# Performance work log

Hardware: AMD Instinct MI355X
Metric: run time of the kernel (lower is better)

Reference implementation:

```python
import jax, jax.numpy as jnp
import numpy as np

T, N, G, H, COV, TW, E = 96, 1024, 128, 512, 8, 8, 32768
D2 = TW * (TW - 1)          # 56, GNN summary width
IN = COV + D2               # 64, exogenous input width


def setup_inputs() -> dict:
    key = jax.random.key(0)
    ks = jax.random.split(key, 32)
    s = 1.0 / np.sqrt(H)

    def u(k, shape):
        return jax.random.uniform(k, shape, jnp.float32, -s, s)

    inp = {
        "input": jax.random.normal(ks[0], (T, 1, IN), jnp.float32),
        "x_nodes": jax.random.normal(ks[1], (T, N, N), jnp.float32),
        "edge_index": jax.random.randint(ks[2], (T, 2, E), 0, N, dtype=jnp.int64),
        "W1": u(ks[3], (N, G)), "b1": u(ks[4], (G,)),
        "W2": u(ks[5], (G, G)), "b2": u(ks[6], (G,)),
        "Wfc": u(ks[7], (G * N, D2)), "bfc": u(ks[8], (D2,)),
        "W_ii": u(ks[9], (IN, H)), "W_gi": u(ks[10], (D2, H)), "W_hi": u(ks[11], (H, H)), "b_i": u(ks[12], (H,)),
        "W_if": u(ks[13], (IN, H)), "W_gf": u(ks[14], (D2, H)), "W_hf": u(ks[15], (H, H)), "b_f": u(ks[16], (H,)),
        "W_ig": u(ks[17], (IN, H)), "W_gg": u(ks[18], (D2, H)), "W_hg": u(ks[19], (H, H)), "b_g": u(ks[20], (H,)),
        "W_io": u(ks[21], (IN, H)), "W_go": u(ks[22], (D2, H)), "W_ho": u(ks[23], (H, H)), "b_o": u(ks[24], (H,)),
    }
    return inp


def reference(input, x_nodes, edge_index,
              W1, b1, W2, b2, Wfc, bfc,
              W_ii, W_gi, W_hi, b_i,
              W_if, W_gf, W_hf, b_f,
              W_ig, W_gg, W_hg, b_g,
              W_io, W_go, W_ho, b_o):
    self_loops = jnp.arange(N, dtype=edge_index.dtype)

    def gcn_conv(x, src, dst, dinv, W, b):
        # GCNConv: out[dst] += d^-1/2[src] d^-1/2[dst] * (x @ W)[src], plus bias
        xw = x @ W                                   # [N, F_out]
        norm = dinv[src] * dinv[dst]                 # [E+N]
        msg = xw[src] * norm[:, None]
        return jax.ops.segment_sum(msg, dst, num_segments=N) + b

    def step(carry, inputs):
        h, c = carry
        x_t, xg, ei = inputs                         # [1,IN], [N,N], [2,E]
        src = jnp.concatenate([ei[0], self_loops])   # add self-loops
        dst = jnp.concatenate([ei[1], self_loops])
        deg = jax.ops.segment_sum(jnp.ones(src.shape, jnp.float32), dst, num_segments=N)
        dinv = jnp.where(deg > 0, jax.lax.rsqrt(jnp.maximum(deg, 1.0)), 0.0)

        xh = jax.nn.relu(gcn_conv(xg, src, dst, dinv, W1, b1))
        xh = gcn_conv(xh, src, dst, dinv, W2, b2)    # [N, G]
        g = jax.nn.relu(xh.reshape(1, -1) @ Wfc + bfc)  # [1, D2]

        i = jax.nn.sigmoid(x_t @ W_ii + g @ W_gi + h @ W_hi + b_i)
        f = jax.nn.sigmoid(x_t @ W_if + g @ W_gf + h @ W_hf + b_f)
        gt = jnp.tanh(x_t @ W_ig + g @ W_gg + h @ W_hg + b_g)
        o = jax.nn.sigmoid(x_t @ W_io + g @ W_go + h @ W_ho + b_o)
        c = f * c + i * gt
        h = o * jnp.tanh(c)
        return (h, c), h

    h0 = jnp.zeros((1, H), jnp.float32)
    c0 = jnp.zeros((1, H), jnp.float32)
    (h, c), outputs = jax.lax.scan(step, (h0, c0), (input, x_nodes, edge_index))
    return outputs, h, c
```

## Files before the change

### kernel.cpp

```cpp
#include <hip/hip_runtime.h>
#include <stdint.h>

#define T_    96
#define TC_   48
#define N_    1024
#define G_    128
#define H_    512
#define E_    32768
#define EN_   33792
#define D2_   56
#define IN_   64
#define KFC_  131072

typedef __bf16 bf16_t;
typedef __bf16 bf16x8 __attribute__((ext_vector_type(8)));
typedef float  f32x4  __attribute__((ext_vector_type(4)));
typedef unsigned short u16;
typedef unsigned long long u64;

struct PtrQuadF { const float* p[4]; };

__device__ inline bf16x8 cvt8(const float* p) {
    const f32x4 a0 = *(const f32x4*)p;
    const f32x4 a1 = *(const f32x4*)(p + 4);
    bf16x8 r;
    r[0] = (bf16_t)a0[0]; r[1] = (bf16_t)a0[1]; r[2] = (bf16_t)a0[2]; r[3] = (bf16_t)a0[3];
    r[4] = (bf16_t)a1[0]; r[5] = (bf16_t)a1[1]; r[6] = (bf16_t)a1[2]; r[7] = (bf16_t)a1[3];
    return r;
}


__global__ __launch_bounds__(1024) void build_kernel(const int* __restrict__ ei,
                                                     int* __restrict__ rowptr_g, int* __restrict__ deg_g,
                                                     u64* __restrict__ ecv) {
    int t = blockIdx.x, tid = threadIdx.x;
    __shared__ int sdeg[N_];
    __shared__ int sa[N_], sb[N_];
    __shared__ int sfill[N_];
    __shared__ float sdinv[N_];
    sdeg[tid] = 0;
    __syncthreads();
    const int* src_p = ei + (size_t)t * 2 * E_;
    const int* dst_p = src_p + E_;
    for (int e = tid; e < E_; e += 1024) atomicAdd(&sdeg[dst_p[e]], 1);
    __syncthreads();
    int d = sdeg[tid] + 1;
    sa[tid] = d;
    __syncthreads();
    int* cur = sa; int* nxt = sb;
    for (int off = 1; off < N_; off <<= 1) {
        int v = cur[tid];
        if (tid >= off) v += cur[tid - off];
        nxt[tid] = v;
        __syncthreads();
        int* tmp = cur; cur = nxt; nxt = tmp;
    }
    int start = cur[tid] - d + t * EN_;
    rowptr_g[t * N_ + tid] = start;
    deg_g[t * N_ + tid] = d;
    sfill[tid] = start;
    sdinv[tid] = rsqrtf((float)d);
    __syncthreads();
    for (int e = tid; e < EN_; e += 1024) {
        int s, dd;
        if (e < E_) { s = src_p[e]; dd = dst_p[e]; }
        else        { s = dd = e - E_; }
        float nrm = sdinv[s] * sdinv[dd];
        int pos = atomicAdd(&sfill[dd], 1);
        ecv[pos] = ((u64)__float_as_uint(nrm) << 32) | (unsigned int)s;
    }
}


__global__ __launch_bounds__(256) void transpose_kernel(const float* __restrict__ src, bf16_t* __restrict__ dst,
                                                        int R, int C, int Cpad) {
    __shared__ bf16_t tile[64][65];
    int rb = blockIdx.x * 64, cb = blockIdx.y * 64;
    int tx = threadIdx.x & 63, ty = threadIdx.x >> 6;
#pragma unroll
    for (int i = 0; i < 16; i++) {
        int r = rb + ty * 16 + i;
        int c = cb + tx;
        float v = 0.f;
        if (r < R && c < C) v = src[(size_t)r * C + c];
        tile[ty * 16 + i][tx] = (bf16_t)v;
    }
    __syncthreads();
#pragma unroll
    for (int i = 0; i < 16; i++) {
        int c = cb + ty * 16 + i;
        int r = rb + tx;
        if (c < Cpad && r < R) dst[(size_t)c * R + r] = tile[tx][ty * 16 + i];
    }
}


__global__ __launch_bounds__(256) void whcvt_kernel(PtrQuadF Wh, bf16_t* __restrict__ dst) {
    int g = blockIdx.y;
    int idx = blockIdx.x * 256 + threadIdx.x;
    dst[(size_t)g * H_ * H_ + idx] = (bf16_t)Wh.p[g][idx];
}


template<bool AF32>
__global__ __launch_bounds__(256) void gemm_g(const void* __restrict__ Ap, const bf16_t* __restrict__ B,
                                              bf16_t* __restrict__ C, const float* __restrict__ bias, int relu,
                                              int K, int Mtiles, size_t sA, size_t sC, int ldc) {
    int t = blockIdx.y;
    int mi = blockIdx.x % Mtiles, ni = blockIdx.x / Mtiles;
    int tid = threadIdx.x;
    int w = tid >> 6, l = tid & 63;
    int wm = w & 1, wn = w >> 1;
    int lm = l & 15, lq = l >> 4;
    f32x4 acc[4][4] = {};
    size_t aO = sA * t + (size_t)(mi * 128 + wm * 64 + lm) * K + lq * 8;
    const bf16_t* Ab16 = (const bf16_t*)Ap + aO;
    const float*  Ab32 = (const float*)Ap + aO;
    const bf16_t* Bb = B + (size_t)(ni * 128 + wn * 64 + lm) * K + lq * 8;
    for (int k0 = 0; k0 < K; k0 += 32) {
        bf16x8 af[4], bfv[4];
#pragma unroll
        for (int i = 0; i < 4; i++) {
            if (AF32) af[i] = cvt8(Ab32 + (size_t)i * 16 * K + k0);
            else      af[i] = *(const bf16x8*)(Ab16 + (size_t)i * 16 * K + k0);
        }
#pragma unroll
        for (int i = 0; i < 4; i++) bfv[i] = *(const bf16x8*)(Bb + (size_t)i * 16 * K + k0);
#pragma unroll
        for (int mt = 0; mt < 4; mt++)
#pragma unroll
            for (int nt = 0; nt < 4; nt++)
                acc[mt][nt] = __builtin_amdgcn_mfma_f32_16x16x32_bf16(af[mt], bfv[nt], acc[mt][nt], 0, 0, 0);
    }
#pragma unroll
    for (int mt = 0; mt < 4; mt++)
#pragma unroll
        for (int nt = 0; nt < 4; nt++) {
            int colg = ni * 128 + wn * 64 + nt * 16 + lm;
            float bv = bias ? bias[colg] : 0.f;
#pragma unroll
            for (int r = 0; r < 4; r++) {
                int row = mi * 128 + wm * 64 + mt * 16 + lq * 4 + r;
                float v = acc[mt][nt][r] + bv;
                if (relu) v = fmaxf(v, 0.f);
                C[sC * t + (size_t)row * ldc + colg] = (bf16_t)v;
            }
        }
}


__device__ inline void spmm_acc(u64 q, const bf16_t* Fb, int l, float& a0, float& a1) {
    int c = (int)(unsigned int)q;
    float wn = __uint_as_float((unsigned int)(q >> 32));
    unsigned int pk = *(const unsigned int*)(Fb + (size_t)c * 128 + 2 * l);
    a0 += wn * __uint_as_float(pk << 16);
    a1 += wn * __uint_as_float(pk & 0xffff0000u);
}

__global__ __launch_bounds__(256) void spmm_kernel(const int* __restrict__ rowptr, const int* __restrict__ deg,
                                                   const u64* __restrict__ ecv, const bf16_t* __restrict__ F,
                                                   const float* __restrict__ bias, int relu,
                                                   bf16_t* __restrict__ out, int t0) {
    int tl = blockIdx.y, t = t0 + tl;
    int w = threadIdx.x >> 6, l = threadIdx.x & 63;
    int r = blockIdx.x * 4 + w;
    int start = rowptr[t * N_ + r];
    int n = deg[t * N_ + r];
    const bf16_t* Fb = F + (size_t)tl * N_ * 128;
    const u64* ep = ecv + start;
    float a0 = 0.f, a1 = 0.f;
    int e = 0;
    for (; e + 4 <= n; e += 4) {
        u64 q0 = ep[e], q1 = ep[e + 1], q2 = ep[e + 2], q3 = ep[e + 3];
        spmm_acc(q0, Fb, l, a0, a1);
        spmm_acc(q1, Fb, l, a0, a1);
        spmm_acc(q2, Fb, l, a0, a1);
        spmm_acc(q3, Fb, l, a0, a1);
    }
    for (; e < n; e++) spmm_acc(ep[e], Fb, l, a0, a1);
    float v0 = a0 + bias[2 * l], v1 = a1 + bias[2 * l + 1];
    if (relu) { v0 = fmaxf(v0, 0.f); v1 = fmaxf(v1, 0.f); }
    bf16_t b0 = (bf16_t)v0, b1 = (bf16_t)v1;
    unsigned int po = (unsigned int)*(u16*)&b0 | ((unsigned int)*(u16*)&b1 << 16);
    *(unsigned int*)((u16*)(out + ((size_t)tl * N_ + r) * 128) + 2 * l) = po;
}


__global__ __launch_bounds__(256) void gfc_kernel(const bf16_t* __restrict__ XH2, const bf16_t* __restrict__ WfcT,
                                                  float* __restrict__ g_acc, int t0) {
    int tid = threadIdx.x;
    int w = tid >> 6, l = tid & 63;
    int lm = l & 15, lq = l >> 4;
    int n = w * 16 + lm;
    size_t k0 = (size_t)blockIdx.x * 1024;
    f32x4 acc[3] = {};
    const bf16_t* Ab = XH2 + (size_t)lm * KFC_ + k0 + lq * 8;
    const bf16_t* Bb = WfcT + (size_t)n * KFC_ + k0 + lq * 8;
    for (int ks = 0; ks < 32; ks++) {
        bf16x8 bfr = *(const bf16x8*)(Bb + ks * 32);
#pragma unroll
        for (int mt = 0; mt < 3; mt++) {
            bf16x8 a = *(const bf16x8*)(Ab + (size_t)(mt * 16) * KFC_ + ks * 32);
            acc[mt] = __builtin_amdgcn_mfma_f32_16x16x32_bf16(a, bfr, acc[mt], 0, 0, 0);
        }
    }
#pragma unroll
    for (int mt = 0; mt < 3; mt++)
#pragma unroll
        for (int r = 0; r < 4; r++) {
            int t = t0 + mt * 16 + lq * 4 + r;
            if (n < D2_) atomicAdd(&g_acc[t * 64 + n], acc[mt][r]);
        }
}


__global__ __launch_bounds__(512) void pregate_kernel(const float* __restrict__ xin, const float* __restrict__ g_acc,
                                                      const float* __restrict__ bfc,
                                                      PtrQuadF Wi, PtrQuadF Wg, PtrQuadF Wb,
                                                      float* __restrict__ out) {
    int gate = blockIdx.x, t = blockIdx.y, j = threadIdx.x;
    __shared__ float gl[D2_];
    __shared__ float xl[IN_];
    if (j < D2_) gl[j] = fmaxf(g_acc[t * 64 + j] + bfc[j], 0.f);
    if (j < IN_) xl[j] = xin[t * IN_ + j];
    __syncthreads();
    const float* wi = Wi.p[gate];
    const float* wg = Wg.p[gate];
    float acc = Wb.p[gate][j];
#pragma unroll 4
    for (int k = 0; k < IN_; k++) acc += xl[k] * wi[k * H_ + j];
#pragma unroll 4
    for (int k = 0; k < D2_; k++) acc += gl[k] * wg[k * H_ + j];
    out[(t * 4 + gate) * H_ + j] = acc;
}


__global__ __launch_bounds__(256) void lstm_kernel(const bf16_t* __restrict__ Whb, const float* __restrict__ pregate,
                                                   u64* __restrict__ h_slot, float* __restrict__ out) {
    int tid = threadIdx.x, bid = blockIdx.x;
    int jl = tid >> 3, kc = tid & 7;
    int j = bid * 32 + jl;
    int k0 = kc * 64;

    uint32_t w[128];
#pragma unroll
    for (int g4 = 0; g4 < 4; g4++) {
        const bf16_t* W = Whb + (size_t)g4 * H_ * H_;
#pragma unroll
        for (int m = 0; m < 32; m++) {
            int k = k0 + 2 * m;
            uint32_t lo = *(const u16*)(W + (size_t)k * H_ + j);
            uint32_t hi = *(const u16*)(W + (size_t)(k + 1) * H_ + j);
            w[g4 * 32 + m] = lo | (hi << 16);
        }
    }

    __shared__ __align__(16) float hl[H_];
    hl[tid] = 0.f;
    hl[tid + 256] = 0.f;
    float c = 0.f;
    __syncthreads();

    for (int step = 0; step < 96; step++) {
        float p0 = 0.f, p1 = 0.f, p2 = 0.f, p3 = 0.f;
        if (kc == 0) {
            const float* pre = pregate + (size_t)step * (4 * H_);
            p0 = pre[0 * H_ + j]; p1 = pre[1 * H_ + j];
            p2 = pre[2 * H_ + j]; p3 = pre[3 * H_ + j];
        }

        float s0 = 0.f, s1 = 0.f, s2 = 0.f, s3 = 0.f;
        const float4* h4 = (const float4*)(hl + k0);
#pragma unroll
        for (int q = 0; q < 16; q++) {
            float4 hq = h4[q];
#pragma unroll
            for (int p = 0; p < 2; p++) {
                float h0 = p ? hq.z : hq.x;
                float h1 = p ? hq.w : hq.y;
                int mi = q * 2 + p;
                uint32_t wv;
                wv = w[0 * 32 + mi];
                s0 += __uint_as_float(wv << 16) * h0 + __uint_as_float(wv & 0xffff0000u) * h1;
                wv = w[1 * 32 + mi];
                s1 += __uint_as_float(wv << 16) * h0 + __uint_as_float(wv & 0xffff0000u) * h1;
                wv = w[2 * 32 + mi];
                s2 += __uint_as_float(wv << 16) * h0 + __uint_as_float(wv & 0xffff0000u) * h1;
                wv = w[3 * 32 + mi];
                s3 += __uint_as_float(wv << 16) * h0 + __uint_as_float(wv & 0xffff0000u) * h1;
            }
        }
        s0 += __shfl_xor(s0, 1); s0 += __shfl_xor(s0, 2); s0 += __shfl_xor(s0, 4);
        s1 += __shfl_xor(s1, 1); s1 += __shfl_xor(s1, 2); s1 += __shfl_xor(s1, 4);
        s2 += __shfl_xor(s2, 1); s2 += __shfl_xor(s2, 2); s2 += __shfl_xor(s2, 4);
        s3 += __shfl_xor(s3, 1); s3 += __shfl_xor(s3, 2); s3 += __shfl_xor(s3, 4);

        if (kc == 0) {
            float ig = 1.f / (1.f + __expf(-(s0 + p0)));
            float fg = 1.f / (1.f + __expf(-(s1 + p1)));
            float gg = tanhf(s2 + p2);
            float og = 1.f / (1.f + __expf(-(s3 + p3)));
            c = fg * c + ig * gg;
            float h = og * tanhf(c);
            if (step < 95) {
                u64 v = ((u64)(unsigned int)(step + 1) << 32) | (u64)__float_as_uint(h);
                __hip_atomic_store(&h_slot[(size_t)step * H_ + j], v, __ATOMIC_RELAXED, __HIP_MEMORY_SCOPE_AGENT);
            }
            out[step * H_ + j] = h;
            if (step == 95) {
                out[96 * H_ + j] = h;
                out[97 * H_ + j] = c;
            }
        }
        if (step < 95) {
            __syncthreads();
            if (tid < 64) {
                unsigned int want = (unsigned int)(step + 1);
                const u64* base = h_slot + (size_t)step * H_ + tid * 8;
                u64 v[8];
                int need = 0xff;
                while (need) {
#pragma unroll
                    for (int s = 0; s < 8; s++)
                        if (need & (1 << s))
                            v[s] = __hip_atomic_load(&base[s], __ATOMIC_RELAXED, __HIP_MEMORY_SCOPE_AGENT);
                    int nd = 0;
#pragma unroll
                    for (int s = 0; s < 8; s++)
                        if ((need & (1 << s)) && (unsigned int)(v[s] >> 32) != want) nd |= 1 << s;
                    need = nd;
                    if (need) __builtin_amdgcn_s_sleep(1);
                }
                float4 f0, f1;
                f0.x = __uint_as_float((unsigned int)v[0]); f0.y = __uint_as_float((unsigned int)v[1]);
                f0.z = __uint_as_float((unsigned int)v[2]); f0.w = __uint_as_float((unsigned int)v[3]);
                f1.x = __uint_as_float((unsigned int)v[4]); f1.y = __uint_as_float((unsigned int)v[5]);
                f1.z = __uint_as_float((unsigned int)v[6]); f1.w = __uint_as_float((unsigned int)v[7]);
                ((float4*)hl)[tid * 2] = f0;
                ((float4*)hl)[tid * 2 + 1] = f1;
            }
            __syncthreads();
        }
    }
}


extern "C" void kernel_launch(void* const* d_in, const int* in_sizes, int n_in,
                              void* d_out, int out_size, void* d_ws, size_t ws_size,
                              hipStream_t stream) {
    const float* xin    = (const float*)d_in[0];
    const float* xnodes = (const float*)d_in[1];
    const int*   ei     = (const int*)d_in[2];
    const float* W1  = (const float*)d_in[3];
    const float* b1  = (const float*)d_in[4];
    const float* W2  = (const float*)d_in[5];
    const float* b2  = (const float*)d_in[6];
    const float* Wfc = (const float*)d_in[7];
    const float* bfc = (const float*)d_in[8];

    PtrQuadF Wi = {{(const float*)d_in[9],  (const float*)d_in[13], (const float*)d_in[17], (const float*)d_in[21]}};
    PtrQuadF Wg = {{(const float*)d_in[10], (const float*)d_in[14], (const float*)d_in[18], (const float*)d_in[22]}};
    PtrQuadF Wh = {{(const float*)d_in[11], (const float*)d_in[15], (const float*)d_in[19], (const float*)d_in[23]}};
    PtrQuadF Wb = {{(const float*)d_in[12], (const float*)d_in[16], (const float*)d_in[20], (const float*)d_in[24]}};

    char* ws = (char*)d_ws;
    size_t off = 0;
    auto alloc = [&](size_t bytes) { void* p = ws + off; off += (bytes + 255) & ~(size_t)255; return p; };

    bf16_t* C1      = (bf16_t*)alloc((size_t)TC_ * N_ * 128 * 2);
    bf16_t* XH1     = (bf16_t*)alloc((size_t)TC_ * N_ * 128 * 2);
    bf16_t* C2      = (bf16_t*)alloc((size_t)TC_ * N_ * 128 * 2);
    bf16_t* XH2     = (bf16_t*)alloc((size_t)TC_ * N_ * 128 * 2);
    u64*    ecv     = (u64*)   alloc((size_t)T_ * EN_ * 8);
    int*    deg     = (int*)   alloc((size_t)T_ * N_ * 4);
    int*    rowptr  = (int*)   alloc((size_t)T_ * N_ * 4);
    bf16_t* W1t     = (bf16_t*)alloc((size_t)128 * 1024 * 2);
    bf16_t* W2t     = (bf16_t*)alloc((size_t)128 * 128 * 2);
    bf16_t* WfcT    = (bf16_t*)alloc((size_t)64 * KFC_ * 2);
    bf16_t* Whb     = (bf16_t*)alloc((size_t)4 * H_ * H_ * 2);
    float*  g_acc   = (float*) alloc((size_t)T_ * 64 * 4);
    float*  pregate = (float*) alloc((size_t)T_ * 4 * H_ * 4);
    u64*    h_slot  = (u64*)   alloc((size_t)T_ * H_ * 8);

    hipMemsetAsync(g_acc, 0, (size_t)T_ * 64 * 4, stream);

    build_kernel<<<T_, 1024, 0, stream>>>(ei, rowptr, deg, ecv);

    transpose_kernel<<<dim3(16, 2), 256, 0, stream>>>(W1, W1t, 1024, 128, 128);
    transpose_kernel<<<dim3(2, 2), 256, 0, stream>>>(W2, W2t, 128, 128, 128);
    transpose_kernel<<<dim3(2048, 1), 256, 0, stream>>>(Wfc, WfcT, KFC_, D2_, 64);
    whcvt_kernel<<<dim3(1024, 4), 256, 0, stream>>>(Wh, Whb);

    for (int c = 0; c < T_ / TC_; c++) {
        int t0 = c * TC_;
        gemm_g<true><<<dim3(8, TC_), 256, 0, stream>>>(
            xnodes + (size_t)t0 * N_ * N_, W1t, C1, nullptr, 0,
            1024, 8, (size_t)N_ * N_, (size_t)N_ * 128, 128);
        spmm_kernel<<<dim3(256, TC_), 256, 0, stream>>>(rowptr, deg, ecv, C1, b1, 1, XH1, t0);
        gemm_g<false><<<dim3(8, TC_), 256, 0, stream>>>(
            XH1, W2t, C2, nullptr, 0,
            128, 8, (size_t)N_ * 128, (size_t)N_ * 128, 128);
        spmm_kernel<<<dim3(256, TC_), 256, 0, stream>>>(rowptr, deg, ecv, C2, b2, 0, XH2, t0);
        gfc_kernel<<<128, 256, 0, stream>>>(XH2, WfcT, g_acc, t0);
    }

    pregate_kernel<<<dim3(4, T_), 512, 0, stream>>>(xin, g_acc, bfc, Wi, Wg, Wb, pregate);

    lstm_kernel<<<16, 256, 0, stream>>>(Whb, pregate, h_slot, (float*)d_out);
}
```

Measured before the change: 1.514 ms.

## Process all timesteps in one pass, merge prep kernels, widen h polling

```diff
diff --git a/kernel.cpp b/kernel.cpp
--- a/kernel.cpp
+++ b/kernel.cpp
@@ -2,7 +2,6 @@
 #include <stdint.h>
 
 #define T_    96
-#define TC_   48
 #define N_    1024
 #define G_    128
 #define H_    512
@@ -72,10 +71,10 @@
 }
 
 
-__global__ __launch_bounds__(256) void transpose_kernel(const float* __restrict__ src, bf16_t* __restrict__ dst,
-                                                        int R, int C, int Cpad) {
+__device__ inline void transpose_tile(const float* __restrict__ src, bf16_t* __restrict__ dst,
+                                      int R, int C, int Cpad, int bx, int by) {
     __shared__ bf16_t tile[64][65];
-    int rb = blockIdx.x * 64, cb = blockIdx.y * 64;
+    int rb = bx * 64, cb = by * 64;
     int tx = threadIdx.x & 63, ty = threadIdx.x >> 6;
 #pragma unroll
     for (int i = 0; i < 16; i++) {
@@ -94,11 +93,24 @@
     }
 }
 
-
-__global__ __launch_bounds__(256) void whcvt_kernel(PtrQuadF Wh, bf16_t* __restrict__ dst) {
-    int g = blockIdx.y;
-    int idx = blockIdx.x * 256 + threadIdx.x;
-    dst[(size_t)g * H_ * H_ + idx] = (bf16_t)Wh.p[g][idx];
+__global__ __launch_bounds__(256) void prep_kernel(const float* __restrict__ W1, const float* __restrict__ W2,
+                                                   const float* __restrict__ Wfc, PtrQuadF Wh,
+                                                   bf16_t* __restrict__ W1t, bf16_t* __restrict__ W2t,
+                                                   bf16_t* __restrict__ WfcT, bf16_t* __restrict__ Whb) {
+    int b = blockIdx.x;
+    if (b < 32) {
+        transpose_tile(W1, W1t, 1024, 128, 128, b & 15, b >> 4);
+    } else if (b < 36) {
+        int bb = b - 32;
+        transpose_tile(W2, W2t, 128, 128, 128, bb & 1, bb >> 1);
+    } else if (b < 2084) {
+        transpose_tile(Wfc, WfcT, KFC_, D2_, 64, b - 36, 0);
+    } else {
+        int idx = (b - 2084) * 256 + threadIdx.x;
+#pragma unroll
+        for (int g = 0; g < 4; g++)
+            Whb[(size_t)g * H_ * H_ + idx] = (bf16_t)Wh.p[g][idx];
+    }
 }
 
 
@@ -160,13 +172,13 @@
 __global__ __launch_bounds__(256) void spmm_kernel(const int* __restrict__ rowptr, const int* __restrict__ deg,
                                                    const u64* __restrict__ ecv, const bf16_t* __restrict__ F,
                                                    const float* __restrict__ bias, int relu,
-                                                   bf16_t* __restrict__ out, int t0) {
-    int tl = blockIdx.y, t = t0 + tl;
+                                                   bf16_t* __restrict__ out) {
+    int t = blockIdx.y;
     int w = threadIdx.x >> 6, l = threadIdx.x & 63;
     int r = blockIdx.x * 4 + w;
     int start = rowptr[t * N_ + r];
     int n = deg[t * N_ + r];
-    const bf16_t* Fb = F + (size_t)tl * N_ * 128;
+    const bf16_t* Fb = F + (size_t)t * N_ * 128;
     const u64* ep = ecv + start;
     float a0 = 0.f, a1 = 0.f;
     int e = 0;
@@ -182,33 +194,33 @@
     if (relu) { v0 = fmaxf(v0, 0.f); v1 = fmaxf(v1, 0.f); }
     bf16_t b0 = (bf16_t)v0, b1 = (bf16_t)v1;
     unsigned int po = (unsigned int)*(u16*)&b0 | ((unsigned int)*(u16*)&b1 << 16);
-    *(unsigned int*)((u16*)(out + ((size_t)tl * N_ + r) * 128) + 2 * l) = po;
+    *(unsigned int*)((u16*)(out + ((size_t)t * N_ + r) * 128) + 2 * l) = po;
 }
 
 
 __global__ __launch_bounds__(256) void gfc_kernel(const bf16_t* __restrict__ XH2, const bf16_t* __restrict__ WfcT,
-                                                  float* __restrict__ g_acc, int t0) {
+                                                  float* __restrict__ g_acc) {
     int tid = threadIdx.x;
     int w = tid >> 6, l = tid & 63;
     int lm = l & 15, lq = l >> 4;
     int n = w * 16 + lm;
-    size_t k0 = (size_t)blockIdx.x * 1024;
-    f32x4 acc[3] = {};
+    size_t k0 = (size_t)blockIdx.x * 512;
+    f32x4 acc[6] = {};
     const bf16_t* Ab = XH2 + (size_t)lm * KFC_ + k0 + lq * 8;
     const bf16_t* Bb = WfcT + (size_t)n * KFC_ + k0 + lq * 8;
-    for (int ks = 0; ks < 32; ks++) {
+    for (int ks = 0; ks < 16; ks++) {
         bf16x8 bfr = *(const bf16x8*)(Bb + ks * 32);
 #pragma unroll
-        for (int mt = 0; mt < 3; mt++) {
+        for (int mt = 0; mt < 6; mt++) {
             bf16x8 a = *(const bf16x8*)(Ab + (size_t)(mt * 16) * KFC_ + ks * 32);
             acc[mt] = __builtin_amdgcn_mfma_f32_16x16x32_bf16(a, bfr, acc[mt], 0, 0, 0);
         }
     }
 #pragma unroll
-    for (int mt = 0; mt < 3; mt++)
+    for (int mt = 0; mt < 6; mt++)
 #pragma unroll
         for (int r = 0; r < 4; r++) {
-            int t = t0 + mt * 16 + lq * 4 + r;
+            int t = mt * 16 + lq * 4 + r;
             if (n < D2_) atomicAdd(&g_acc[t * 64 + n], acc[mt][r]);
         }
 }
@@ -314,31 +326,19 @@
         }
         if (step < 95) {
             __syncthreads();
-            if (tid < 64) {
-                unsigned int want = (unsigned int)(step + 1);
-                const u64* base = h_slot + (size_t)step * H_ + tid * 8;
-                u64 v[8];
-                int need = 0xff;
-                while (need) {
-#pragma unroll
-                    for (int s = 0; s < 8; s++)
-                        if (need & (1 << s))
-                            v[s] = __hip_atomic_load(&base[s], __ATOMIC_RELAXED, __HIP_MEMORY_SCOPE_AGENT);
-                    int nd = 0;
-#pragma unroll
-                    for (int s = 0; s < 8; s++)
-                        if ((need & (1 << s)) && (unsigned int)(v[s] >> 32) != want) nd |= 1 << s;
-                    need = nd;
-                    if (need) __builtin_amdgcn_s_sleep(1);
-                }
-                float4 f0, f1;
-                f0.x = __uint_as_float((unsigned int)v[0]); f0.y = __uint_as_float((unsigned int)v[1]);
-                f0.z = __uint_as_float((unsigned int)v[2]); f0.w = __uint_as_float((unsigned int)v[3]);
-                f1.x = __uint_as_float((unsigned int)v[4]); f1.y = __uint_as_float((unsigned int)v[5]);
-                f1.z = __uint_as_float((unsigned int)v[6]); f1.w = __uint_as_float((unsigned int)v[7]);
-                ((float4*)hl)[tid * 2] = f0;
-                ((float4*)hl)[tid * 2 + 1] = f1;
+            unsigned int want = (unsigned int)(step + 1);
+            const u64* base = h_slot + (size_t)step * H_ + tid * 2;
+            u64 v0, v1;
+            for (;;) {
+                v0 = __hip_atomic_load(&base[0], __ATOMIC_RELAXED, __HIP_MEMORY_SCOPE_AGENT);
+                v1 = __hip_atomic_load(&base[1], __ATOMIC_RELAXED, __HIP_MEMORY_SCOPE_AGENT);
+                if (((unsigned int)(v0 >> 32) == want) & ((unsigned int)(v1 >> 32) == want)) break;
+                __builtin_amdgcn_s_sleep(1);
             }
+            float2 f;
+            f.x = __uint_as_float((unsigned int)v0);
+            f.y = __uint_as_float((unsigned int)v1);
+            ((float2*)hl)[tid] = f;
             __syncthreads();
         }
     }
@@ -367,10 +367,8 @@
     size_t off = 0;
     auto alloc = [&](size_t bytes) { void* p = ws + off; off += (bytes + 255) & ~(size_t)255; return p; };
 
-    bf16_t* C1      = (bf16_t*)alloc((size_t)TC_ * N_ * 128 * 2);
-    bf16_t* XH1     = (bf16_t*)alloc((size_t)TC_ * N_ * 128 * 2);
-    bf16_t* C2      = (bf16_t*)alloc((size_t)TC_ * N_ * 128 * 2);
-    bf16_t* XH2     = (bf16_t*)alloc((size_t)TC_ * N_ * 128 * 2);
+    bf16_t* bufA    = (bf16_t*)alloc((size_t)T_ * N_ * 128 * 2);
+    bf16_t* bufB    = (bf16_t*)alloc((size_t)T_ * N_ * 128 * 2);
     u64*    ecv     = (u64*)   alloc((size_t)T_ * EN_ * 8);
     int*    deg     = (int*)   alloc((size_t)T_ * N_ * 4);
     int*    rowptr  = (int*)   alloc((size_t)T_ * N_ * 4);
@@ -385,24 +383,17 @@
     hipMemsetAsync(g_acc, 0, (size_t)T_ * 64 * 4, stream);
 
     build_kernel<<<T_, 1024, 0, stream>>>(ei, rowptr, deg, ecv);
-
-    transpose_kernel<<<dim3(16, 2), 256, 0, stream>>>(W1, W1t, 1024, 128, 128);
-    transpose_kernel<<<dim3(2, 2), 256, 0, stream>>>(W2, W2t, 128, 128, 128);
-    transpose_kernel<<<dim3(2048, 1), 256, 0, stream>>>(Wfc, WfcT, KFC_, D2_, 64);
-    whcvt_kernel<<<dim3(1024, 4), 256, 0, stream>>>(Wh, Whb);
-
-    for (int c = 0; c < T_ / TC_; c++) {
-        int t0 = c * TC_;
-        gemm_g<true><<<dim3(8, TC_), 256, 0, stream>>>(
-            xnodes + (size_t)t0 * N_ * N_, W1t, C1, nullptr, 0,
-            1024, 8, (size_t)N_ * N_, (size_t)N_ * 128, 128);
-        spmm_kernel<<<dim3(256, TC_), 256, 0, stream>>>(rowptr, deg, ecv, C1, b1, 1, XH1, t0);
-        gemm_g<false><<<dim3(8, TC_), 256, 0, stream>>>(
-            XH1, W2t, C2, nullptr, 0,
-            128, 8, (size_t)N_ * 128, (size_t)N_ * 128, 128);
-        spmm_kernel<<<dim3(256, TC_), 256, 0, stream>>>(rowptr, deg, ecv, C2, b2, 0, XH2, t0);
-        gfc_kernel<<<128, 256, 0, stream>>>(XH2, WfcT, g_acc, t0);
-    }
+    prep_kernel<<<3108, 256, 0, stream>>>(W1, W2, Wfc, Wh, W1t, W2t, WfcT, Whb);
+
+    gemm_g<true><<<dim3(8, T_), 256, 0, stream>>>(
+        xnodes, W1t, bufA, nullptr, 0,
+        1024, 8, (size_t)N_ * N_, (size_t)N_ * 128, 128);
+    spmm_kernel<<<dim3(256, T_), 256, 0, stream>>>(rowptr, deg, ecv, bufA, b1, 1, bufB);
+    gemm_g<false><<<dim3(8, T_), 256, 0, stream>>>(
+        bufB, W2t, bufA, nullptr, 0,
+        128, 8, (size_t)N_ * 128, (size_t)N_ * 128, 128);
+    spmm_kernel<<<dim3(256, T_), 256, 0, stream>>>(rowptr, deg, ecv, bufA, b2, 0, bufB);
+    gfc_kernel<<<256, 256, 0, stream>>>(bufB, WfcT, g_acc);
 
     pregate_kernel<<<dim3(4, T_), 512, 0, stream>>>(xin, g_acc, bfc, Wi, Wg, Wb, pregate);
 
```

Measured after the change: 1.324 ms. -12.6%, faster.
